# Kernel tuning notes

Measured on AMD Instinct MI355X. Metric: run time of the kernel, lower is better.

## Reference

```python
import jax, jax.numpy as jnp
import numpy as np

N_CLASSES = 9
N_GROUPS = 2


def setup_inputs() -> dict:
    key = jax.random.key(0)
    k1, k2 = jax.random.split(key)
    N = 16_777_216  # number of samples
    preds = jax.random.randint(k1, (N,), 0, N_CLASSES, dtype=jnp.int32)
    attrs = jax.random.randint(k2, (N,), 0, N_GROUPS, dtype=jnp.int32)
    return {"preds": preds, "attrs": attrs}


def reference(preds, attrs):
    # Fused histogram: flatten (class, group) -> single bin id in [0, 18)
    flat = preds * N_GROUPS + attrs  # [N]
    counts = jax.ops.segment_sum(
        jnp.ones_like(flat, dtype=jnp.float32), flat,
        num_segments=N_CLASSES * N_GROUPS,
    ).reshape(N_CLASSES, N_GROUPS)  # [9, 2] histogram

    n_attr_1 = jnp.sum(attrs != 0).astype(jnp.float32)
    n_attr_0 = jnp.float32(attrs.shape[0]) - n_attr_1

    diff = counts[:, 0] / n_attr_0 - counts[:, 1] / n_attr_1  # [9]
    return jnp.sum(diff * diff)
```

## Files before the change

### kernel.cpp

```cpp
#include <hip/hip_runtime.h>


#define N_CLASSES 9
#define N_GROUPS 2
#define NBINS (N_CLASSES * N_GROUPS)
#define GRID_BLOCKS 2048
#define CHUNK 31

__global__ __launch_bounds__(256) void spd_hist_kernel(
    const int* __restrict__ preds,
    const int* __restrict__ attrs,
    unsigned int* __restrict__ partials,
    int n4, int n)
{
    __shared__ unsigned int lh0[N_CLASSES];
    __shared__ unsigned int lh1[N_CLASSES];
    if (threadIdx.x < N_CLASSES) { lh0[threadIdx.x] = 0u; lh1[threadIdx.x] = 0u; }
    __syncthreads();

    unsigned int cnt[N_CLASSES];
    #pragma unroll
    for (int p = 0; p < N_CLASSES; ++p) cnt[p] = 0u;

    const int4* __restrict__ p4 = (const int4*)preds;
    const int4* __restrict__ a4 = (const int4*)attrs;
    const int stride = gridDim.x * blockDim.x;

    int i = blockIdx.x * blockDim.x + threadIdx.x;
    while (i < n4) {
        unsigned long long acc0 = 0ull, acc1 = 0ull;
        int lim = CHUNK;
        for (; i < n4 && lim; i += stride, --lim) {
            int4 p = p4[i];
            int4 a = a4[i];
            {
                unsigned long long inc = 1ull << (7 * p.x);
                acc0 += (a.x == 0) ? inc : 0ull;
                acc1 += (a.x == 0) ? 0ull : inc;
            }
            {
                unsigned long long inc = 1ull << (7 * p.y);
                acc0 += (a.y == 0) ? inc : 0ull;
                acc1 += (a.y == 0) ? 0ull : inc;
            }
            {
                unsigned long long inc = 1ull << (7 * p.z);
                acc0 += (a.z == 0) ? inc : 0ull;
                acc1 += (a.z == 0) ? 0ull : inc;
            }
            {
                unsigned long long inc = 1ull << (7 * p.w);
                acc0 += (a.w == 0) ? inc : 0ull;
                acc1 += (a.w == 0) ? 0ull : inc;
            }
        }
        #pragma unroll
        for (int p = 0; p < N_CLASSES; ++p) {
            unsigned int c0 = (unsigned int)(acc0 >> (7 * p)) & 127u;
            unsigned int c1 = (unsigned int)(acc1 >> (7 * p)) & 127u;
            cnt[p] += c0 | (c1 << 16);
        }
    }

    if (blockIdx.x == 0) {
        for (int t = n4 * 4 + (int)threadIdx.x; t < n; t += (int)blockDim.x)
            cnt[preds[t]] += (attrs[t] == 0) ? 1u : 0x10000u;
    }

    #pragma unroll
    for (int m = 1; m < 64; m <<= 1) {
        #pragma unroll
        for (int p = 0; p < N_CLASSES; ++p)
            cnt[p] += __shfl_xor(cnt[p], m, 64);
    }

    if ((threadIdx.x & 63) == 0) {
        #pragma unroll
        for (int p = 0; p < N_CLASSES; ++p) {
            atomicAdd(&lh0[p], cnt[p] & 0xFFFFu);
            atomicAdd(&lh1[p], cnt[p] >> 16);
        }
    }
    __syncthreads();

    if (threadIdx.x < NBINS) {
        int c = threadIdx.x >> 1;
        unsigned int v = (threadIdx.x & 1) ? lh1[c] : lh0[c];
        partials[blockIdx.x * NBINS + threadIdx.x] = v;
    }
}

__global__ __launch_bounds__(1024) void spd_finalize_kernel(
    const unsigned int* __restrict__ partials,
    float* __restrict__ out, int nblocks, double n_total)
{
    __shared__ double counts[NBINS];
    const int tid = threadIdx.x;

    if (tid < NBINS * 32) {
        const int bin = tid >> 5;
        const int j = tid & 31;
        unsigned int s = 0u;
        for (int b = j; b < nblocks; b += 32)
            s += partials[b * NBINS + bin];
        #pragma unroll
        for (int m = 1; m < 32; m <<= 1)
            s += __shfl_xor(s, m, 32);
        if (j == 0) counts[bin] = (double)s;
    }
    __syncthreads();

    if (tid == 0) {
        double n1 = 0.0;
        #pragma unroll
        for (int c = 0; c < N_CLASSES; ++c)
            n1 += counts[c * N_GROUPS + 1];
        double n0 = n_total - n1;
        double acc = 0.0;
        #pragma unroll
        for (int c = 0; c < N_CLASSES; ++c) {
            double d = counts[c * N_GROUPS] / n0 - counts[c * N_GROUPS + 1] / n1;
            acc += d * d;
        }
        out[0] = (float)acc;
    }
}

extern "C" void kernel_launch(void* const* d_in, const int* in_sizes, int n_in,
                              void* d_out, int out_size, void* d_ws, size_t ws_size,
                              hipStream_t stream)
{
    const int* preds = (const int*)d_in[0];
    const int* attrs = (const int*)d_in[1];
    const int n = in_sizes[0];

    unsigned int* partials = (unsigned int*)d_ws;

    const int n4 = n / 4;
    const int block = 256;
    int grid = (n4 + block - 1) / block;
    if (grid > GRID_BLOCKS) grid = GRID_BLOCKS;
    int max_grid = (int)(ws_size / (NBINS * sizeof(unsigned int)));
    if (grid > max_grid) grid = max_grid;
    if (grid < 1) grid = 1;

    spd_hist_kernel<<<grid, block, 0, stream>>>(preds, attrs, partials, n4, n);
    spd_finalize_kernel<<<1, 1024, 0, stream>>>(partials, (float*)d_out, grid, (double)n);
}
```

Before: 156.2 us.

## Batch eight int4 loads per thread in block-contiguous spans with 512-thread blocks

The grid-stride loop with one load pair per iteration becomes a block-contiguous span loop. Each thread issues eight int4 loads of preds and eight of attrs up front before accumulating, which raises memory-level parallelism. Block size goes from 256 to 512 and the grid is sized from the per-block span, giving 1024 blocks for this input. The finalize reduction loop is also unrolled; register pressure from the sixteen int4 values may lower occupancy.

```diff
diff --git a/kernel.cpp b/kernel.cpp
--- a/kernel.cpp
+++ b/kernel.cpp
@@ -4,10 +4,9 @@
 #define N_CLASSES 9
 #define N_GROUPS 2
 #define NBINS (N_CLASSES * N_GROUPS)
-#define GRID_BLOCKS 2048
-#define CHUNK 31
+#define ITEMS 8
 
-__global__ __launch_bounds__(256) void spd_hist_kernel(
+__global__ __launch_bounds__(512) void spd_hist_kernel(
     const int* __restrict__ preds,
     const int* __restrict__ attrs,
     unsigned int* __restrict__ partials,
@@ -24,36 +23,71 @@
 
     const int4* __restrict__ p4 = (const int4*)preds;
     const int4* __restrict__ a4 = (const int4*)attrs;
-    const int stride = gridDim.x * blockDim.x;
 
-    int i = blockIdx.x * blockDim.x + threadIdx.x;
-    while (i < n4) {
+    const int span = (int)blockDim.x * ITEMS;
+    for (int S = blockIdx.x * span; S < n4; S += gridDim.x * span) {
+        const int s = S + (int)threadIdx.x;
         unsigned long long acc0 = 0ull, acc1 = 0ull;
-        int lim = CHUNK;
-        for (; i < n4 && lim; i += stride, --lim) {
-            int4 p = p4[i];
-            int4 a = a4[i];
-            {
-                unsigned long long inc = 1ull << (7 * p.x);
-                acc0 += (a.x == 0) ? inc : 0ull;
-                acc1 += (a.x == 0) ? 0ull : inc;
+
+        if (S + span <= n4) {
+            int4 p[ITEMS], a[ITEMS];
+            #pragma unroll
+            for (int k = 0; k < ITEMS; ++k) p[k] = p4[s + k * (int)blockDim.x];
+            #pragma unroll
+            for (int k = 0; k < ITEMS; ++k) a[k] = a4[s + k * (int)blockDim.x];
+            #pragma unroll
+            for (int k = 0; k < ITEMS; ++k) {
+                {
+                    unsigned long long inc = 1ull << (7 * p[k].x);
+                    acc0 += (a[k].x == 0) ? inc : 0ull;
+                    acc1 += (a[k].x == 0) ? 0ull : inc;
+                }
+                {
+                    unsigned long long inc = 1ull << (7 * p[k].y);
+                    acc0 += (a[k].y == 0) ? inc : 0ull;
+                    acc1 += (a[k].y == 0) ? 0ull : inc;
+                }
+                {
+                    unsigned long long inc = 1ull << (7 * p[k].z);
+                    acc0 += (a[k].z == 0) ? inc : 0ull;
+                    acc1 += (a[k].z == 0) ? 0ull : inc;
+                }
+                {
+                    unsigned long long inc = 1ull << (7 * p[k].w);
+                    acc0 += (a[k].w == 0) ? inc : 0ull;
+                    acc1 += (a[k].w == 0) ? 0ull : inc;
+                }
             }
-            {
-                unsigned long long inc = 1ull << (7 * p.y);
-                acc0 += (a.y == 0) ? inc : 0ull;
-                acc1 += (a.y == 0) ? 0ull : inc;
-            }
-            {
-                unsigned long long inc = 1ull << (7 * p.z);
-                acc0 += (a.z == 0) ? inc : 0ull;
-                acc1 += (a.z == 0) ? 0ull : inc;
-            }
-            {
-                unsigned long long inc = 1ull << (7 * p.w);
-                acc0 += (a.w == 0) ? inc : 0ull;
-                acc1 += (a.w == 0) ? 0ull : inc;
+        } else {
+            for (int k = 0; k < ITEMS; ++k) {
+                const int idx = s + k * (int)blockDim.x;
+                if (idx < n4) {
+                    int4 pp = p4[idx];
+                    int4 aa = a4[idx];
+                    {
+                        unsigned long long inc = 1ull << (7 * pp.x);
+                        acc0 += (aa.x == 0) ? inc : 0ull;
+                        acc1 += (aa.x == 0) ? 0ull : inc;
+                    }
+                    {
+                        unsigned long long inc = 1ull << (7 * pp.y);
+                        acc0 += (aa.y == 0) ? inc : 0ull;
+                        acc1 += (aa.y == 0) ? 0ull : inc;
+                    }
+                    {
+                        unsigned long long inc = 1ull << (7 * pp.z);
+                        acc0 += (aa.z == 0) ? inc : 0ull;
+                        acc1 += (aa.z == 0) ? 0ull : inc;
+                    }
+                    {
+                        unsigned long long inc = 1ull << (7 * pp.w);
+                        acc0 += (aa.w == 0) ? inc : 0ull;
+                        acc1 += (aa.w == 0) ? 0ull : inc;
+                    }
+                }
             }
         }
+
         #pragma unroll
         for (int p = 0; p < N_CLASSES; ++p) {
             unsigned int c0 = (unsigned int)(acc0 >> (7 * p)) & 127u;
@@ -101,6 +135,7 @@
         const int bin = tid >> 5;
         const int j = tid & 31;
         unsigned int s = 0u;
+        #pragma unroll 8
         for (int b = j; b < nblocks; b += 32)
             s += partials[b * NBINS + bin];
         #pragma unroll
@@ -137,9 +172,10 @@
     unsigned int* partials = (unsigned int*)d_ws;
 
     const int n4 = n / 4;
-    const int block = 256;
-    int grid = (n4 + block - 1) / block;
-    if (grid > GRID_BLOCKS) grid = GRID_BLOCKS;
+    const int block = 512;
+    const int per_block = block * ITEMS;
+    int grid = (n4 + per_block - 1) / per_block;
+    if (grid > 2048) grid = 2048;
     int max_grid = (int)(ws_size / (NBINS * sizeof(unsigned int)));
     if (grid > max_grid) grid = max_grid;
     if (grid < 1) grid = 1;
```

New measurement: 151.8 us. -2.9%, faster.

## Double-buffer vectorized loads in registers with block-tiled spans and nontemporal hints

Applied to the files above, without the earlier changes.

Restructures the histogram loop so each block processes contiguous spans of ITEMS vec4 loads per thread, prefetching the next span into a second register buffer while counting the current one. Loads use nontemporal hints and the grid is reduced to 1024 blocks. The intent is more outstanding memory requests per thread to hide latency on a bandwidth-bound scan. It raises register pressure and adds a separate tail path.

```diff
diff --git a/kernel.cpp b/kernel.cpp
--- a/kernel.cpp
+++ b/kernel.cpp
@@ -4,10 +4,20 @@
 #define N_CLASSES 9
 #define N_GROUPS 2
 #define NBINS (N_CLASSES * N_GROUPS)
-#define GRID_BLOCKS 2048
-#define CHUNK 31
+#define ITEMS 4
+#define BLOCK 256
 
-__global__ __launch_bounds__(256) void spd_hist_kernel(
+typedef int v4i __attribute__((ext_vector_type(4)));
+
+__device__ __forceinline__ void acc_item(int pv, int av,
+                                         unsigned long long& acc0,
+                                         unsigned long long& acc1) {
+    unsigned long long inc = 1ull << (7 * pv);
+    acc0 += (av == 0) ? inc : 0ull;
+    acc1 += (av == 0) ? 0ull : inc;
+}
+
+__global__ __launch_bounds__(BLOCK) void spd_hist_kernel(
     const int* __restrict__ preds,
     const int* __restrict__ attrs,
     unsigned int* __restrict__ partials,
@@ -22,48 +32,79 @@
     #pragma unroll
     for (int p = 0; p < N_CLASSES; ++p) cnt[p] = 0u;
 
-    const int4* __restrict__ p4 = (const int4*)preds;
-    const int4* __restrict__ a4 = (const int4*)attrs;
-    const int stride = gridDim.x * blockDim.x;
+    const v4i* __restrict__ p4 = (const v4i*)preds;
+    const v4i* __restrict__ a4 = (const v4i*)attrs;
+    const int tid = (int)threadIdx.x;
 
-    int i = blockIdx.x * blockDim.x + threadIdx.x;
-    while (i < n4) {
+    const int span = BLOCK * ITEMS;
+    const int stride = gridDim.x * span;
+
+    v4i pb[2][ITEMS], ab[2][ITEMS];
+
+    int S = blockIdx.x * span;
+    int buf = 0;
+    bool have = (S + span <= n4);
+
+    if (have) {
+        const int s = S + tid;
+        #pragma unroll
+        for (int k = 0; k < ITEMS; ++k) pb[0][k] = __builtin_nontemporal_load(p4 + s + k * BLOCK);
+        #pragma unroll
+        for (int k = 0; k < ITEMS; ++k) ab[0][k] = __builtin_nontemporal_load(a4 + s + k * BLOCK);
+    }
+
+    while (have) {
+        const int Snext = S + stride;
+        const bool havenext = (Snext + span <= n4);
+        if (havenext) {
+            const int s = Snext + tid;
+            #pragma unroll
+            for (int k = 0; k < ITEMS; ++k) pb[buf ^ 1][k] = __builtin_nontemporal_load(p4 + s + k * BLOCK);
+            #pragma unroll
+            for (int k = 0; k < ITEMS; ++k) ab[buf ^ 1][k] = __builtin_nontemporal_load(a4 + s + k * BLOCK);
+        }
+
         unsigned long long acc0 = 0ull, acc1 = 0ull;
-        int lim = CHUNK;
-        for (; i < n4 && lim; i += stride, --lim) {
-            int4 p = p4[i];
-            int4 a = a4[i];
-            {
-                unsigned long long inc = 1ull << (7 * p.x);
-                acc0 += (a.x == 0) ? inc : 0ull;
-                acc1 += (a.x == 0) ? 0ull : inc;
-            }
-            {
-                unsigned long long inc = 1ull << (7 * p.y);
-                acc0 += (a.y == 0) ? inc : 0ull;
-                acc1 += (a.y == 0) ? 0ull : inc;
-            }
-            {
-                unsigned long long inc = 1ull << (7 * p.z);
-                acc0 += (a.z == 0) ? inc : 0ull;
-                acc1 += (a.z == 0) ? 0ull : inc;
-            }
-            {
-                unsigned long long inc = 1ull << (7 * p.w);
-                acc0 += (a.w == 0) ? inc : 0ull;
-                acc1 += (a.w == 0) ? 0ull : inc;
+        #pragma unroll
+        for (int k = 0; k < ITEMS; ++k) {
+            acc_item(pb[buf][k].x, ab[buf][k].x, acc0, acc1);
+            acc_item(pb[buf][k].y, ab[buf][k].y, acc0, acc1);
+            acc_item(pb[buf][k].z, ab[buf][k].z, acc0, acc1);
+            acc_item(pb[buf][k].w, ab[buf][k].w, acc0, acc1);
+        }
+        #pragma unroll
+        for (int p = 0; p < N_CLASSES; ++p) {
+            cnt[p] += ((unsigned int)(acc0 >> (7 * p)) & 127u)
+                    | (((unsigned int)(acc1 >> (7 * p)) & 127u) << 16);
+        }
+
+        buf ^= 1;
+        S = Snext;
+        have = havenext;
+    }
+
+    if (S < n4) {
+        unsigned long long acc0 = 0ull, acc1 = 0ull;
+        for (int k = 0; k < ITEMS; ++k) {
+            const int idx = S + tid + k * BLOCK;
+            if (idx < n4) {
+                v4i pp = p4[idx];
+                v4i aa = a4[idx];
+                acc_item(pp.x, aa.x, acc0, acc1);
+                acc_item(pp.y, aa.y, acc0, acc1);
+                acc_item(pp.z, aa.z, acc0, acc1);
+                acc_item(pp.w, aa.w, acc0, acc1);
             }
         }
         #pragma unroll
         for (int p = 0; p < N_CLASSES; ++p) {
-            unsigned int c0 = (unsigned int)(acc0 >> (7 * p)) & 127u;
-            unsigned int c1 = (unsigned int)(acc1 >> (7 * p)) & 127u;
-            cnt[p] += c0 | (c1 << 16);
+            cnt[p] += ((unsigned int)(acc0 >> (7 * p)) & 127u)
+                    | (((unsigned int)(acc1 >> (7 * p)) & 127u) << 16);
         }
     }
 
     if (blockIdx.x == 0) {
-        for (int t = n4 * 4 + (int)threadIdx.x; t < n; t += (int)blockDim.x)
+        for (int t = n4 * 4 + tid; t < n; t += BLOCK)
             cnt[preds[t]] += (attrs[t] == 0) ? 1u : 0x10000u;
     }
 
@@ -74,7 +115,7 @@
             cnt[p] += __shfl_xor(cnt[p], m, 64);
     }
 
-    if ((threadIdx.x & 63) == 0) {
+    if ((tid & 63) == 0) {
         #pragma unroll
         for (int p = 0; p < N_CLASSES; ++p) {
             atomicAdd(&lh0[p], cnt[p] & 0xFFFFu);
@@ -83,10 +124,10 @@
     }
     __syncthreads();
 
-    if (threadIdx.x < NBINS) {
-        int c = threadIdx.x >> 1;
-        unsigned int v = (threadIdx.x & 1) ? lh1[c] : lh0[c];
-        partials[blockIdx.x * NBINS + threadIdx.x] = v;
+    if (tid < NBINS) {
+        int c = tid >> 1;
+        unsigned int v = (tid & 1) ? lh1[c] : lh0[c];
+        partials[blockIdx.x * NBINS + tid] = v;
     }
 }
 
@@ -101,6 +142,7 @@
         const int bin = tid >> 5;
         const int j = tid & 31;
         unsigned int s = 0u;
+        #pragma unroll 8
         for (int b = j; b < nblocks; b += 32)
             s += partials[b * NBINS + bin];
         #pragma unroll
@@ -137,13 +179,13 @@
     unsigned int* partials = (unsigned int*)d_ws;
 
     const int n4 = n / 4;
-    const int block = 256;
-    int grid = (n4 + block - 1) / block;
-    if (grid > GRID_BLOCKS) grid = GRID_BLOCKS;
+    const int span = BLOCK * ITEMS;
+    int grid = (n4 + span - 1) / span;
+    if (grid > 1024) grid = 1024;
     int max_grid = (int)(ws_size / (NBINS * sizeof(unsigned int)));
     if (grid > max_grid) grid = max_grid;
     if (grid < 1) grid = 1;
 
-    spd_hist_kernel<<<grid, block, 0, stream>>>(preds, attrs, partials, n4, n);
+    spd_hist_kernel<<<grid, BLOCK, 0, stream>>>(preds, attrs, partials, n4, n);
     spd_finalize_kernel<<<1, 1024, 0, stream>>>(partials, (float*)d_out, grid, (double)n);
 }
```

Result: no change. 157.0 us (median of 2 runs) (+0.5%).
